# Performance work log

Measured on AMD Instinct MI355X. Metric: run time of the kernel, lower is better.

## Reference

```python
import jax, jax.numpy as jnp
import numpy as np

NEG = -1000000.0

def setup_inputs() -> dict:
    key = jax.random.key(0)
    ks = jax.random.split(key, 7)
    B, Lq, Lk, Dq, Dk, Dv, H = 4, 256, 1024, 512, 512, 512, 256
    return {
        "query": jax.random.normal(ks[0], (B, Lq, Dq), dtype=jnp.float32),
        "key": jax.random.normal(ks[1], (B, Lk, Dk), dtype=jnp.float32),
        "value": jax.random.normal(ks[2], (B, Lk, Dv), dtype=jnp.float32),
        "valid_len": jax.random.randint(ks[3], (B,), 1, Lk + 1),
        "Wq": jax.random.normal(ks[4], (Dq, H), dtype=jnp.float32) * (1.0 / np.sqrt(Dq)),
        "Wk": jax.random.normal(ks[5], (Dk, H), dtype=jnp.float32) * (1.0 / np.sqrt(Dk)),
        "wv": jax.random.normal(ks[6], (H,), dtype=jnp.float32) * (1.0 / np.sqrt(H)),
    }

def reference(query, key, value, valid_len, Wq, Wk, wv):
    # projections: [B,Lq,H], [B,Lk,H]
    q = jnp.einsum("bqd,dh->bqh", query, Wq)
    k = jnp.einsum("bkd,dh->bkh", key, Wk)
    # broadcast-add + tanh: [B,Lq,Lk,H]
    features = jnp.tanh(q[:, :, None, :] + k[:, None, :, :])
    # score projection to scalar: [B,Lq,Lk]
    score = jnp.einsum("bqkh,h->bqk", features, wv)
    # masked softmax over keys (valid_len per batch, broadcast over queries)
    Lk = key.shape[1]
    mask = jnp.arange(Lk)[None, None, :] < valid_len[:, None, None]
    score = jnp.where(mask, score, NEG)
    attn = jax.nn.softmax(score, axis=-1)
    # weighted sum of values: [B,Lq,Dv]  (dropout is identity in eval)
    return jnp.einsum("bqk,bkv->bqv", attn, value)
```

## Files before the change

kernel.cpp:

```cpp
#include <hip/hip_runtime.h>

#define TWO_LOG2E 2.8853900817779268f
#define LOG2E     1.4426950408889634f

__global__ __launch_bounds__(256) void proj_kernel(
    const float* __restrict__ query, const float* __restrict__ key,
    const float* __restrict__ Wq, const float* __restrict__ Wk,
    const int* __restrict__ valid_len,
    float* __restrict__ Eq, float* __restrict__ EkT)
{
    __shared__ float lds[64 * 66];
    float (*As)[68] = (float(*)[68])lds;
    float (*Bs)[64] = (float(*)[64])(lds + 16 * 68);

    const int tid = threadIdx.x;
    const int tx = tid & 15, ty = tid >> 4;
    const int m0 = blockIdx.y * 64, n0 = blockIdx.x * 64;
    const bool isq = (m0 < 1024);

    if (!isq) {
        const int krow0 = m0 - 1024;
        const int b = krow0 >> 10, kk0 = krow0 & 1023;
        if (kk0 >= valid_len[b]) return;
    }

    const float* Ap = isq ? (query + (size_t)m0 * 512)
                          : (key + (size_t)(m0 - 1024) * 512);
    const float* Bp = isq ? Wq : Wk;

    const int lr = tid >> 2, lc = (tid & 3) * 4;
    const int br = tid >> 4, bc = (tid & 15) * 4;

    float4 av = *(const float4*)(Ap + (size_t)lr * 512 + lc);
    float4 bv = *(const float4*)(Bp + (size_t)br * 256 + n0 + bc);

    float c[4][4] = {};

    for (int kt = 0; kt < 512; kt += 16) {
        __syncthreads();
        As[lc + 0][lr] = av.x; As[lc + 1][lr] = av.y;
        As[lc + 2][lr] = av.z; As[lc + 3][lr] = av.w;
        *(float4*)&Bs[br][bc] = bv;
        __syncthreads();
        if (kt + 16 < 512) {
            av = *(const float4*)(Ap + (size_t)lr * 512 + kt + 16 + lc);
            bv = *(const float4*)(Bp + (size_t)(kt + 16 + br) * 256 + n0 + bc);
        }
        #pragma unroll
        for (int k = 0; k < 16; ++k) {
            const float4 a = *(const float4*)&As[k][ty * 4];
            const float4 bb = *(const float4*)&Bs[k][tx * 4];
            const float ar[4] = {a.x, a.y, a.z, a.w};
            const float brr[4] = {bb.x, bb.y, bb.z, bb.w};
            #pragma unroll
            for (int i = 0; i < 4; ++i)
                #pragma unroll
                for (int j = 0; j < 4; ++j)
                    c[i][j] = fmaf(ar[i], brr[j], c[i][j]);
        }
    }

    if (isq) {
        #pragma unroll
        for (int i = 0; i < 4; ++i) {
            float4 o;
            o.x = __builtin_amdgcn_exp2f(c[i][0] * TWO_LOG2E);
            o.y = __builtin_amdgcn_exp2f(c[i][1] * TWO_LOG2E);
            o.z = __builtin_amdgcn_exp2f(c[i][2] * TWO_LOG2E);
            o.w = __builtin_amdgcn_exp2f(c[i][3] * TWO_LOG2E);
            *(float4*)(Eq + (size_t)(m0 + ty * 4 + i) * 256 + n0 + tx * 4) = o;
        }
    } else {
        __syncthreads();
        float (*Ct)[66] = (float(*)[66])lds;
        #pragma unroll
        for (int i = 0; i < 4; ++i)
            #pragma unroll
            for (int j = 0; j < 4; ++j)
                Ct[tx * 4 + j][ty * 4 + i] =
                    __builtin_amdgcn_exp2f(c[i][j] * TWO_LOG2E);
        __syncthreads();
        const int krow0 = m0 - 1024;
        const int b = krow0 >> 10, kk0 = krow0 & 1023;
        const int hr = tid >> 2, mc = (tid & 3) * 4;
        #pragma unroll
        for (int rep = 0; rep < 4; ++rep) {
            const int m = mc + rep * 16;
            float4 o;
            o.x = Ct[hr][m]; o.y = Ct[hr][m + 1];
            o.z = Ct[hr][m + 2]; o.w = Ct[hr][m + 3];
            *(float4*)(EkT + (size_t)(b * 256 + n0 + hr) * 1024 + kk0 + m) = o;
        }
    }
}

__global__ __launch_bounds__(1024) void score_softmax_kernel(
    const float* __restrict__ Eq, const float* __restrict__ EkT,
    const float* __restrict__ wv, const int* __restrict__ valid_len,
    float* __restrict__ attn)
{
    __shared__ float wv_s[256];
    __shared__ float eq4_s[256 * 4];
    __shared__ float red[16][4];

    const int tid = threadIdx.x;
    const int b = blockIdx.x >> 6;
    const int q0 = (blockIdx.x & 63) << 2;

    const int vlen = valid_len[b];
    const int k = tid;
    const bool v = (k < vlen);

    if (tid < 256) wv_s[tid] = wv[tid];
    {
        const int q = tid >> 8, h = tid & 255;
        eq4_s[h * 4 + q] = Eq[(size_t)(b * 256 + q0 + q) * 256 + h];
    }
    __syncthreads();

    float acc[4] = {};
    float cw = 0.f;

    if (v) {
        const float* ekp = EkT + (size_t)(b * 256) * 1024 + k;
        #pragma unroll 8
        for (int h = 0; h < 256; ++h) {
            const float ek = ekp[(size_t)h * 1024];
            const float4 eq = *(const float4*)&eq4_s[h * 4];
            const float w = wv_s[h];
            cw += w;
            acc[0] = fmaf(w, __builtin_amdgcn_rcpf(fmaf(eq.x, ek, 1.f)), acc[0]);
            acc[1] = fmaf(w, __builtin_amdgcn_rcpf(fmaf(eq.y, ek, 1.f)), acc[1]);
            acc[2] = fmaf(w, __builtin_amdgcn_rcpf(fmaf(eq.z, ek, 1.f)), acc[2]);
            acc[3] = fmaf(w, __builtin_amdgcn_rcpf(fmaf(eq.w, ek, 1.f)), acc[3]);
        }
    }

    float s[4], m[4];
    #pragma unroll
    for (int q = 0; q < 4; ++q) {
        s[q] = fmaf(-2.f, acc[q], cw);
        m[q] = v ? s[q] : -1e30f;
    }
    #pragma unroll
    for (int o = 32; o; o >>= 1) {
        #pragma unroll
        for (int q = 0; q < 4; ++q) m[q] = fmaxf(m[q], __shfl_xor(m[q], o));
    }
    const int wid = tid >> 6;
    if ((tid & 63) == 0) {
        #pragma unroll
        for (int q = 0; q < 4; ++q) red[wid][q] = m[q];
    }
    __syncthreads();
    #pragma unroll
    for (int q = 0; q < 4; ++q) {
        float mm = red[0][q];
        #pragma unroll
        for (int w = 1; w < 16; ++w) mm = fmaxf(mm, red[w][q]);
        m[q] = mm;
    }
    __syncthreads();

    float p[4], l[4];
    #pragma unroll
    for (int q = 0; q < 4; ++q) {
        p[q] = v ? __builtin_amdgcn_exp2f((s[q] - m[q]) * LOG2E) : 0.f;
        l[q] = p[q];
    }
    #pragma unroll
    for (int o = 32; o; o >>= 1) {
        #pragma unroll
        for (int q = 0; q < 4; ++q) l[q] += __shfl_xor(l[q], o);
    }
    if ((tid & 63) == 0) {
        #pragma unroll
        for (int q = 0; q < 4; ++q) red[wid][q] = l[q];
    }
    __syncthreads();
    #pragma unroll
    for (int q = 0; q < 4; ++q) {
        float ss = red[0][q];
        #pragma unroll
        for (int w = 1; w < 16; ++w) ss += red[w][q];
        const float rl = __builtin_amdgcn_rcpf(ss);
        attn[(size_t)(b * 256 + q0 + q) * 1024 + k] = p[q] * rl;
    }
}

__global__ __launch_bounds__(256) void pv_kernel(
    const float* __restrict__ attn, const float* __restrict__ value,
    const int* __restrict__ valid_len,
    float* __restrict__ out)
{
    __shared__ float As[32][34];
    __shared__ float Bs[32][64];

    const int tid = threadIdx.x;
    const int b = blockIdx.z;
    const int m0 = blockIdx.y * 32, n0 = blockIdx.x * 64;
    const float* A = attn + ((size_t)b * 256 + m0) * 1024;
    const float* B = value + (size_t)b * 1024 * 512;

    const int kend = (valid_len[b] + 31) & ~31;

    const int tx = tid & 15, ty = tid >> 4;
    const int lr = tid >> 3, lc = (tid & 7) * 4;
    const int br = tid >> 4, bc = (tid & 15) * 4;

    float4 av  = *(const float4*)(A + (size_t)lr * 1024 + lc);
    float4 bv0 = *(const float4*)(B + (size_t)br * 512 + n0 + bc);
    float4 bv1 = *(const float4*)(B + (size_t)(br + 16) * 512 + n0 + bc);

    float c[2][4] = {};

    for (int kt = 0; kt < kend; kt += 32) {
        __syncthreads();
        As[lc + 0][lr] = av.x; As[lc + 1][lr] = av.y;
        As[lc + 2][lr] = av.z; As[lc + 3][lr] = av.w;
        *(float4*)&Bs[br][bc] = bv0;
        *(float4*)&Bs[br + 16][bc] = bv1;
        __syncthreads();
        if (kt + 32 < kend) {
            av  = *(const float4*)(A + (size_t)lr * 1024 + kt + 32 + lc);
            bv0 = *(const float4*)(B + (size_t)(kt + 32 + br) * 512 + n0 + bc);
            bv1 = *(const float4*)(B + (size_t)(kt + 48 + br) * 512 + n0 + bc);
        }
        #pragma unroll
        for (int k = 0; k < 32; ++k) {
            const float2 a = *(const float2*)&As[k][ty * 2];
            const float4 bb = *(const float4*)&Bs[k][tx * 4];
            c[0][0] = fmaf(a.x, bb.x, c[0][0]);
            c[0][1] = fmaf(a.x, bb.y, c[0][1]);
            c[0][2] = fmaf(a.x, bb.z, c[0][2]);
            c[0][3] = fmaf(a.x, bb.w, c[0][3]);
            c[1][0] = fmaf(a.y, bb.x, c[1][0]);
            c[1][1] = fmaf(a.y, bb.y, c[1][1]);
            c[1][2] = fmaf(a.y, bb.z, c[1][2]);
            c[1][3] = fmaf(a.y, bb.w, c[1][3]);
        }
    }

    #pragma unroll
    for (int i = 0; i < 2; ++i) {
        float4 o;
        o.x = c[i][0]; o.y = c[i][1]; o.z = c[i][2]; o.w = c[i][3];
        *(float4*)(out + (size_t)b * 256 * 512 +
                   (size_t)(m0 + ty * 2 + i) * 512 + n0 + tx * 4) = o;
    }
}

extern "C" void kernel_launch(void* const* d_in, const int* in_sizes, int n_in,
                              void* d_out, int out_size, void* d_ws, size_t ws_size,
                              hipStream_t stream)
{
    const float* query = (const float*)d_in[0];
    const float* key   = (const float*)d_in[1];
    const float* value = (const float*)d_in[2];
    const int*   vlen  = (const int*)d_in[3];
    const float* Wq    = (const float*)d_in[4];
    const float* Wk    = (const float*)d_in[5];
    const float* wv    = (const float*)d_in[6];
    float* out = (float*)d_out;

    float* Eq   = (float*)d_ws;
    float* EkT  = Eq + 262144;
    float* attn = EkT + 1048576;

    hipLaunchKernelGGL(proj_kernel, dim3(4, 80), dim3(256), 0, stream,
                       query, key, Wq, Wk, vlen, Eq, EkT);
    hipLaunchKernelGGL(score_softmax_kernel, dim3(256), dim3(1024), 0, stream,
                       Eq, EkT, wv, vlen, attn);
    hipLaunchKernelGGL(pv_kernel, dim3(8, 8, 4), dim3(256), 0, stream,
                       attn, value, vlen, out);
}
```

Measured before the change: 85.41 us.

## Replace FP32 SIMT projection GEMM with split-bf16 MFMA and prep kernels

Adds prep kernels that split the query/key rows and the transposed weights into bf16 hi/lo pairs. The projection GEMM then runs on MFMA 16x16x32 bf16 instructions, using three products per tile to recover near-fp32 accuracy. Eq is now stored transposed so the score kernel can load it with float4. This moves the projection from FP32 FMAs onto matrix cores, at the cost of two extra launches, extra workspace traffic for the bf16 copies, and one-wave blocks that read operands straight from global memory with no LDS reuse.

```diff
diff --git a/kernel.cpp b/kernel.cpp
--- a/kernel.cpp
+++ b/kernel.cpp
@@ -1,101 +1,141 @@
 #include <hip/hip_runtime.h>
+
+typedef __attribute__((ext_vector_type(8))) short short8v;
+typedef __attribute__((ext_vector_type(4))) float float4v;
+typedef unsigned int uint;
 
 #define TWO_LOG2E 2.8853900817779268f
 #define LOG2E     1.4426950408889634f
 
-__global__ __launch_bounds__(256) void proj_kernel(
+__device__ inline uint rne_bf16(float x) {
+    uint u = __float_as_uint(x);
+    return (u + 0x7fffu + ((u >> 16) & 1u)) >> 16;
+}
+__device__ inline uint pack_hi_lo(float a0, float a1, uint& lo_pack) {
+    const uint h0 = rne_bf16(a0), h1 = rne_bf16(a1);
+    const float f0 = __uint_as_float(h0 << 16), f1 = __uint_as_float(h1 << 16);
+    const float l0 = a0 - f0, l1 = a1 - f1;
+    lo_pack = (rne_bf16(l1) << 16) | rne_bf16(l0);
+    return (h1 << 16) | h0;
+}
+
+__global__ __launch_bounds__(256) void prep_a(
     const float* __restrict__ query, const float* __restrict__ key,
+    const int* __restrict__ vlen,
+    ushort* __restrict__ A_hi, ushort* __restrict__ A_lo)
+{
+    const int t = blockIdx.x * 256 + threadIdx.x;
+    const int row = t >> 6;
+    const int cg = (t & 63) * 8;
+    if (row >= 1024) {
+        const int kr = (row - 1024) & 1023, b = (row - 1024) >> 10;
+        if ((kr & ~63) >= vlen[b]) return;
+    }
+    const float* src = (row < 1024) ? (query + (size_t)row * 512 + cg)
+                                    : (key + (size_t)(row - 1024) * 512 + cg);
+    const float4 x0 = *(const float4*)src;
+    const float4 x1 = *(const float4*)(src + 4);
+    uint h0, h1, h2, h3, l0, l1, l2, l3;
+    h0 = pack_hi_lo(x0.x, x0.y, l0);
+    h1 = pack_hi_lo(x0.z, x0.w, l1);
+    h2 = pack_hi_lo(x1.x, x1.y, l2);
+    h3 = pack_hi_lo(x1.z, x1.w, l3);
+    *(uint4*)(A_hi + (size_t)row * 512 + cg) = make_uint4(h0, h1, h2, h3);
+    *(uint4*)(A_lo + (size_t)row * 512 + cg) = make_uint4(l0, l1, l2, l3);
+}
+
+__global__ __launch_bounds__(256) void prep_w(
     const float* __restrict__ Wq, const float* __restrict__ Wk,
+    ushort* __restrict__ WT_hi, ushort* __restrict__ WT_lo)
+{
+    const int t = blockIdx.x * 256 + threadIdx.x;
+    const int n = t & 255;
+    const int kg = ((t >> 8) & 63) * 8;
+    const int w = t >> 14;
+    const float* W = w ? Wk : Wq;
+    float x[8];
+    #pragma unroll
+    for (int i = 0; i < 8; ++i) x[i] = W[(size_t)(kg + i) * 256 + n];
+    uint h0, h1, h2, h3, l0, l1, l2, l3;
+    h0 = pack_hi_lo(x[0], x[1], l0);
+    h1 = pack_hi_lo(x[2], x[3], l1);
+    h2 = pack_hi_lo(x[4], x[5], l2);
+    h3 = pack_hi_lo(x[6], x[7], l3);
+    const size_t off = ((size_t)w * 256 + n) * 512 + kg;
+    *(uint4*)(WT_hi + off) = make_uint4(h0, h1, h2, h3);
+    *(uint4*)(WT_lo + off) = make_uint4(l0, l1, l2, l3);
+}
+
+#define LOADF(s, kbase) { const int ko = (kbase) + half * 8;                              \
+    _Pragma("unroll") for (int f = 0; f < 4; ++f) {                                       \
+        ah##s[f] = *(const short8v*)(a_h + (size_t)(f * 16) * 512 + ko);                  \
+        al##s[f] = *(const short8v*)(a_l + (size_t)(f * 16) * 512 + ko);                  \
+        bh##s[f] = *(const short8v*)(wt_h + (size_t)(f * 16) * 512 + ko);                 \
+        bl##s[f] = *(const short8v*)(wt_l + (size_t)(f * 16) * 512 + ko); } }
+
+#define MFMAS(s)                                                                          \
+    _Pragma("unroll") for (int mf = 0; mf < 4; ++mf)                                      \
+    _Pragma("unroll") for (int nf = 0; nf < 4; ++nf) {                                    \
+        acc[mf][nf] = __builtin_amdgcn_mfma_f32_16x16x32_bf16(ah##s[mf], bh##s[nf], acc[mf][nf], 0, 0, 0); \
+        acc[mf][nf] = __builtin_amdgcn_mfma_f32_16x16x32_bf16(ah##s[mf], bl##s[nf], acc[mf][nf], 0, 0, 0); \
+        acc[mf][nf] = __builtin_amdgcn_mfma_f32_16x16x32_bf16(al##s[mf], bh##s[nf], acc[mf][nf], 0, 0, 0); }
+
+__global__ __launch_bounds__(64) void proj_mfma(
+    const ushort* __restrict__ A_hi, const ushort* __restrict__ A_lo,
+    const ushort* __restrict__ WT_hi, const ushort* __restrict__ WT_lo,
     const int* __restrict__ valid_len,
-    float* __restrict__ Eq, float* __restrict__ EkT)
-{
-    __shared__ float lds[64 * 66];
-    float (*As)[68] = (float(*)[68])lds;
-    float (*Bs)[64] = (float(*)[64])(lds + 16 * 68);
-
-    const int tid = threadIdx.x;
-    const int tx = tid & 15, ty = tid >> 4;
-    const int m0 = blockIdx.y * 64, n0 = blockIdx.x * 64;
+    float* __restrict__ EqT, float* __restrict__ EkT)
+{
+    const int lane = threadIdx.x;
+    const int n0 = blockIdx.x * 64;
+    const int m0 = blockIdx.y * 64;
     const bool isq = (m0 < 1024);
-
+    int b = 0, kk0 = 0;
     if (!isq) {
-        const int krow0 = m0 - 1024;
-        const int b = krow0 >> 10, kk0 = krow0 & 1023;
+        kk0 = (m0 - 1024) & 1023;
+        b = (m0 - 1024) >> 10;
         if (kk0 >= valid_len[b]) return;
     }
-
-    const float* Ap = isq ? (query + (size_t)m0 * 512)
-                          : (key + (size_t)(m0 - 1024) * 512);
-    const float* Bp = isq ? Wq : Wk;
-
-    const int lr = tid >> 2, lc = (tid & 3) * 4;
-    const int br = tid >> 4, bc = (tid & 15) * 4;
-
-    float4 av = *(const float4*)(Ap + (size_t)lr * 512 + lc);
-    float4 bv = *(const float4*)(Bp + (size_t)br * 256 + n0 + bc);
-
-    float c[4][4] = {};
-
-    for (int kt = 0; kt < 512; kt += 16) {
-        __syncthreads();
-        As[lc + 0][lr] = av.x; As[lc + 1][lr] = av.y;
-        As[lc + 2][lr] = av.z; As[lc + 3][lr] = av.w;
-        *(float4*)&Bs[br][bc] = bv;
-        __syncthreads();
-        if (kt + 16 < 512) {
-            av = *(const float4*)(Ap + (size_t)lr * 512 + kt + 16 + lc);
-            bv = *(const float4*)(Bp + (size_t)(kt + 16 + br) * 256 + n0 + bc);
-        }
-        #pragma unroll
-        for (int k = 0; k < 16; ++k) {
-            const float4 a = *(const float4*)&As[k][ty * 4];
-            const float4 bb = *(const float4*)&Bs[k][tx * 4];
-            const float ar[4] = {a.x, a.y, a.z, a.w};
-            const float brr[4] = {bb.x, bb.y, bb.z, bb.w};
+    const int r = lane & 15, half = lane >> 4;
+    const size_t wsel = isq ? 0 : (size_t)256 * 512;
+    const ushort* wt_h = WT_hi + wsel + (size_t)(n0 + r) * 512;
+    const ushort* wt_l = WT_lo + wsel + (size_t)(n0 + r) * 512;
+    const ushort* a_h = A_hi + (size_t)(m0 + r) * 512;
+    const ushort* a_l = A_lo + (size_t)(m0 + r) * 512;
+
+    float4v acc[4][4] = {{{0.f}}};
+    short8v ah0[4], al0[4], bh0[4], bl0[4];
+    short8v ah1[4], al1[4], bh1[4], bl1[4];
+
+    LOADF(0, 0);
+    for (int kt = 0; kt < 512; kt += 64) {
+        LOADF(1, kt + 32);
+        MFMAS(0);
+        if (kt + 64 < 512) LOADF(0, kt + 64);
+        MFMAS(1);
+    }
+
+    #pragma unroll
+    for (int mf = 0; mf < 4; ++mf) {
+        #pragma unroll
+        for (int nf = 0; nf < 4; ++nf) {
+            float4v e;
             #pragma unroll
             for (int i = 0; i < 4; ++i)
-                #pragma unroll
-                for (int j = 0; j < 4; ++j)
-                    c[i][j] = fmaf(ar[i], brr[j], c[i][j]);
+                e[i] = __builtin_amdgcn_exp2f(acc[mf][nf][i] * TWO_LOG2E);
+            if (isq) {
+                *(float4v*)(EqT + (size_t)(n0 + nf * 16 + r) * 1024 +
+                            m0 + mf * 16 + half * 4) = e;
+            } else {
+                *(float4v*)(EkT + (size_t)(b * 256 + n0 + nf * 16 + r) * 1024 +
+                            kk0 + mf * 16 + half * 4) = e;
+            }
         }
     }
-
-    if (isq) {
-        #pragma unroll
-        for (int i = 0; i < 4; ++i) {
-            float4 o;
-            o.x = __builtin_amdgcn_exp2f(c[i][0] * TWO_LOG2E);
-            o.y = __builtin_amdgcn_exp2f(c[i][1] * TWO_LOG2E);
-            o.z = __builtin_amdgcn_exp2f(c[i][2] * TWO_LOG2E);
-            o.w = __builtin_amdgcn_exp2f(c[i][3] * TWO_LOG2E);
-            *(float4*)(Eq + (size_t)(m0 + ty * 4 + i) * 256 + n0 + tx * 4) = o;
-        }
-    } else {
-        __syncthreads();
-        float (*Ct)[66] = (float(*)[66])lds;
-        #pragma unroll
-        for (int i = 0; i < 4; ++i)
-            #pragma unroll
-            for (int j = 0; j < 4; ++j)
-                Ct[tx * 4 + j][ty * 4 + i] =
-                    __builtin_amdgcn_exp2f(c[i][j] * TWO_LOG2E);
-        __syncthreads();
-        const int krow0 = m0 - 1024;
-        const int b = krow0 >> 10, kk0 = krow0 & 1023;
-        const int hr = tid >> 2, mc = (tid & 3) * 4;
-        #pragma unroll
-        for (int rep = 0; rep < 4; ++rep) {
-            const int m = mc + rep * 16;
-            float4 o;
-            o.x = Ct[hr][m]; o.y = Ct[hr][m + 1];
-            o.z = Ct[hr][m + 2]; o.w = Ct[hr][m + 3];
-            *(float4*)(EkT + (size_t)(b * 256 + n0 + hr) * 1024 + kk0 + m) = o;
-        }
-    }
 }
 
 __global__ __launch_bounds__(1024) void score_softmax_kernel(
-    const float* __restrict__ Eq, const float* __restrict__ EkT,
+    const float* __restrict__ EqT, const float* __restrict__ EkT,
     const float* __restrict__ wv, const int* __restrict__ valid_len,
     float* __restrict__ attn)
 {
@@ -111,10 +151,10 @@
     const int k = tid;
     const bool v = (k < vlen);
 
-    if (tid < 256) wv_s[tid] = wv[tid];
-    {
-        const int q = tid >> 8, h = tid & 255;
-        eq4_s[h * 4 + q] = Eq[(size_t)(b * 256 + q0 + q) * 256 + h];
+    if (tid < 256) {
+        wv_s[tid] = wv[tid];
+        *(float4*)&eq4_s[tid * 4] =
+            *(const float4*)(EqT + (size_t)tid * 1024 + b * 256 + q0);
     }
     __syncthreads();
 
@@ -263,14 +303,22 @@
     const float* wv    = (const float*)d_in[6];
     float* out = (float*)d_out;
 
-    float* Eq   = (float*)d_ws;
-    float* EkT  = Eq + 262144;
-    float* attn = EkT + 1048576;
-
-    hipLaunchKernelGGL(proj_kernel, dim3(4, 80), dim3(256), 0, stream,
-                       query, key, Wq, Wk, vlen, Eq, EkT);
+    float*  EqT   = (float*)d_ws;
+    float*  EkT   = EqT + 262144;
+    float*  attn  = EkT + 1048576;
+    ushort* A_hi  = (ushort*)(attn + 1048576);
+    ushort* A_lo  = A_hi + 2621440;
+    ushort* WT_hi = A_lo + 2621440;
+    ushort* WT_lo = WT_hi + 262144;
+
+    hipLaunchKernelGGL(prep_w, dim3(128), dim3(256), 0, stream,
+                       Wq, Wk, WT_hi, WT_lo);
+    hipLaunchKernelGGL(prep_a, dim3(1280), dim3(256), 0, stream,
+                       query, key, vlen, A_hi, A_lo);
+    hipLaunchKernelGGL(proj_mfma, dim3(4, 80), dim3(64), 0, stream,
+                       A_hi, A_lo, WT_hi, WT_lo, vlen, EqT, EkT);
     hipLaunchKernelGGL(score_softmax_kernel, dim3(256), dim3(1024), 0, stream,
-                       Eq, EkT, wv, vlen, attn);
+                       EqT, EkT, wv, vlen, attn);
     hipLaunchKernelGGL(pv_kernel, dim3(8, 8, 4), dim3(256), 0, stream,
                        attn, value, vlen, out);
 }
```

After: 84.06 us. No clear change (-1.6%).
